# Kernel tuning notes

Measured on AMD Instinct MI355X. Metric: run time of the kernel, lower is better.

The kernel has to match this reference:

```python
import jax, jax.numpy as jnp
import numpy as np

EPS = 1e-5

def rmsnorm(x, g):
    var = jnp.mean(jnp.square(x), axis=-1, keepdims=True)
    return x * jax.lax.rsqrt(var + EPS) * g

def setup_inputs() -> dict:
    key = jax.random.key(0)
    ks = jax.random.split(key, 8)
    B, S, T, D = 2, 2048, 2048, 1024
    H, HKV, HD = 16, 4, 64
    std = 0.02
    return {
        "x": jax.random.normal(ks[0], (B, S, D), jnp.float32),
        "kv": jax.random.normal(ks[1], (B, T, D), jnp.float32),
        "wq": jax.random.normal(ks[2], (H * HD, D), jnp.float32) * std,
        "wk": jax.random.normal(ks[3], (HKV * HD, D), jnp.float32) * std,
        "wv": jax.random.normal(ks[4], (HKV * HD, D), jnp.float32) * std,
        "wo": jax.random.normal(ks[5], (D, H * HD), jnp.float32) * std,
        "gq": jnp.ones((D,), jnp.float32),
        "gkv": jnp.ones((D,), jnp.float32),
    }

def reference(x, kv, wq, wk, wv, wo, gq, gkv):
    B, S, D = x.shape
    T = kv.shape[1]
    H, HKV, HD = 16, 4, 64
    R = H // HKV  # heads per kv group
    xn = rmsnorm(x, gq)
    kvn = rmsnorm(kv, gkv)
    # projections
    q = (xn @ wq.T).reshape(B, S, HKV, R, HD)   # grouped query heads
    k = (kvn @ wk.T).reshape(B, T, HKV, HD)
    v = (kvn @ wv.T).reshape(B, T, HKV, HD)
    scale = 1.0 / jnp.sqrt(jnp.float32(HD))
    # block-mask is None -> full dense cross attention; GQA via broadcast einsum
    scores = jnp.einsum('bsgrd,btgd->bgrst', q, k) * scale  # [B,HKV,R,S,T]
    probs = jax.nn.softmax(scores, axis=-1)
    out = jnp.einsum('bgrst,btgd->bsgrd', probs, v)  # [B,S,HKV,R,HD]
    out = out.reshape(B, S, H * HD) @ wo.T
    return x + out
```

## Files before the change

kernel.cpp:

```cpp
#include <hip/hip_runtime.h>

#define DEV __device__ __forceinline__

typedef __attribute__((ext_vector_type(8))) short frag8;
typedef __attribute__((ext_vector_type(8))) _Float16 h8;
typedef __attribute__((ext_vector_type(4))) float f32x4;

DEV unsigned short f2bf(float f) {
  union { float f; unsigned int u; } v; v.f = f;
  unsigned int r = v.u + 0x7fffu + ((v.u >> 16) & 1u);
  return (unsigned short)(r >> 16);
}

DEV unsigned short f2h(float f) {
  union { _Float16 h[2]; unsigned short u[2]; } v;
  v.h[0] = (_Float16)f;
  return v.u[0];
}

DEV unsigned int pack2h(float a, float b) {
  union { __fp16 __attribute__((ext_vector_type(2))) p; unsigned int u; } v;
  v.p = __builtin_amdgcn_cvt_pkrtz(a, b);
  return v.u;
}

DEV void async_load16(const void* g, void* l) {
  __builtin_amdgcn_global_load_lds(
      (const __attribute__((address_space(1))) void*)g,
      (__attribute__((address_space(3))) void*)l,
      16, 0, 0);
}

__global__ __launch_bounds__(256) void fused_cast(const float* __restrict__ wq,
                                                  const float* __restrict__ wk,
                                                  const float* __restrict__ wv,
                                                  const float* __restrict__ wo,
                                                  unsigned short* __restrict__ wqb,
                                                  unsigned short* __restrict__ wkvb,
                                                  unsigned short* __restrict__ wob,
                                                  float qscale) {
  const int b = blockIdx.x;
  const float* src;
  unsigned short* dst;
  float sc = 1.0f;
  int base;
  if (b < 1024) { src = wq; dst = wqb; sc = qscale; base = b; }
  else if (b < 1280) { src = wk; dst = wkvb; base = b - 1024; }
  else if (b < 1536) { src = wv; dst = wkvb + 262144; base = b - 1280; }
  else { src = wo; dst = wob; base = b - 1536; }
  const int i = (base * 256 + threadIdx.x) * 4;
  float4 v = *(const float4*)&src[i];
  ushort4 o;
  o.x = f2bf(v.x * sc); o.y = f2bf(v.y * sc);
  o.z = f2bf(v.z * sc); o.w = f2bf(v.w * sc);
  *(ushort4*)&dst[i] = o;
}

__global__ __launch_bounds__(256) void rmsnorm2(const float* __restrict__ x,
                                                const float* __restrict__ kv,
                                                const float* __restrict__ gq,
                                                const float* __restrict__ gkv,
                                                unsigned short* __restrict__ xn,
                                                unsigned short* __restrict__ kvn) {
  int row = blockIdx.x;
  const int tid = threadIdx.x;
  const float* src;
  const float* g;
  unsigned short* dst;
  if (row < 4096) { src = x; g = gq; dst = xn; }
  else { row -= 4096; src = kv; g = gkv; dst = kvn; }
  const float* xr = src + (size_t)row * 1024;
  float4 v = *(const float4*)&xr[tid * 4];
  float ss = v.x * v.x + v.y * v.y + v.z * v.z + v.w * v.w;
  ss += __shfl_xor(ss, 32); ss += __shfl_xor(ss, 16);
  ss += __shfl_xor(ss, 8);  ss += __shfl_xor(ss, 4);
  ss += __shfl_xor(ss, 2);  ss += __shfl_xor(ss, 1);
  __shared__ float red[4];
  if ((tid & 63) == 0) red[tid >> 6] = ss;
  __syncthreads();
  float tot = red[0] + red[1] + red[2] + red[3];
  float inv = rsqrtf(tot * (1.0f / 1024.0f) + 1e-5f);
  float4 gv = *(const float4*)&g[tid * 4];
  ushort4 o;
  o.x = f2bf(v.x * inv * gv.x); o.y = f2bf(v.y * inv * gv.y);
  o.z = f2bf(v.z * inv * gv.z); o.w = f2bf(v.w * inv * gv.w);
  *(ushort4*)&dst[(size_t)row * 1024 + tid * 4] = o;
}

template <int BM, int BN, int MODE>
__global__ __launch_bounds__(256) void gemm_bt(const unsigned short* __restrict__ A,
                                               const unsigned short* __restrict__ W,
                                               void* __restrict__ out,
                                               const float* __restrict__ resid,
                                               unsigned short* __restrict__ out2,
                                               int M, int N, int K) {
  constexpr int MI = BM / 32, NI = BN / 32;
  constexpr int PA = BM / 32, PB = BN / 32;
  __shared__ unsigned short Al[2][2][BM * 32];
  __shared__ unsigned short Bl[2][2][BN * 32];
  const int tid = threadIdx.x;
  const int w = tid >> 6, l = tid & 63;
  const int quad = l >> 4, ln = l & 15;
  const int m0 = blockIdx.y * BM, n0 = blockIdx.x * BN;
  const int wm0 = (w >> 1) * (MI * 16), wn0 = (w & 1) * (NI * 16);
  const int r4 = l >> 2;
  const int c4 = (l & 3) * 8;

  f32x4 acc[MI][NI] = {};

  auto stage = [&](int buf, int kk) {
#pragma unroll
    for (int j = 0; j < PA; ++j) {
      const int idx = w * PA + j;
      const int p = idx / (BM / 16), c = idx % (BM / 16);
      async_load16(A + (size_t)(m0 + c * 16 + r4) * K + kk + p * 32 + c4,
                   &Al[buf][p][c * 512]);
    }
#pragma unroll
    for (int j = 0; j < PB; ++j) {
      const int idx = w * PB + j;
      const int p = idx / (BN / 16), c = idx % (BN / 16);
      async_load16(W + (size_t)(n0 + c * 16 + r4) * K + kk + p * 32 + c4,
                   &Bl[buf][p][c * 512]);
    }
  };

  stage(0, 0);
  const int iters = K >> 6;
#pragma unroll 2
  for (int it = 0; it < iters; ++it) {
    const int buf = it & 1;
    __syncthreads();
    if (it + 1 < iters) stage(buf ^ 1, (it + 1) << 6);
#pragma unroll
    for (int kc = 0; kc < 2; ++kc) {
      frag8 af[MI], bfr[NI];
#pragma unroll
      for (int mi = 0; mi < MI; ++mi)
        af[mi] = *(const frag8*)&Al[buf][kc][(wm0 + mi * 16 + ln) * 32 + quad * 8];
#pragma unroll
      for (int ni = 0; ni < NI; ++ni)
        bfr[ni] = *(const frag8*)&Bl[buf][kc][(wn0 + ni * 16 + ln) * 32 + quad * 8];
#pragma unroll
      for (int mi = 0; mi < MI; ++mi)
#pragma unroll
        for (int ni = 0; ni < NI; ++ni)
          acc[mi][ni] = __builtin_amdgcn_mfma_f32_16x16x32_bf16(af[mi], bfr[ni], acc[mi][ni], 0, 0, 0);
    }
  }

#pragma unroll
  for (int mi = 0; mi < MI; ++mi) {
#pragma unroll
    for (int ni = 0; ni < NI; ++ni) {
#pragma unroll
      for (int r = 0; r < 4; ++r) {
        const int row = m0 + wm0 + mi * 16 + quad * 4 + r;
        const int col = n0 + wn0 + ni * 16 + ln;
        const float v = acc[mi][ni][r];
        if (MODE == 0) {
          ((unsigned short*)out)[(size_t)row * N + col] = f2bf(v);
        } else if (MODE == 2) {
          const size_t idx = (size_t)row * N + col;
          ((float*)out)[idx] = resid[idx] + v;
        } else {
          if (col < 256) {
            ((unsigned short*)out)[(size_t)row * 256 + col] = f2bf(v);
          } else {
            const int c2 = col - 256, gg = c2 >> 6, dd = c2 & 63;
            const int bb = row >> 11, t = row & 2047;
            out2[((size_t)((bb * 4 + gg) * 64 + dd) << 11) + t] = f2h(v);
          }
        }
      }
    }
  }
}

__global__ __launch_bounds__(256) void flash_attn(const unsigned short* __restrict__ q,
                                                  const unsigned short* __restrict__ k,
                                                  const unsigned short* __restrict__ vT,
                                                  unsigned short* __restrict__ att) {
  __shared__ unsigned short KV[2][4][64 * 32];
  __shared__ unsigned short P[4 * 32 * 72];
  __shared__ float Lbuf[128];

  const int tid = threadIdx.x;
  const int w = tid >> 6, l = tid & 63;
  const int quad = l >> 4, ln = l & 15;
  const int s0 = blockIdx.x * 128;
  const int h = blockIdx.y, g = h >> 2, b = blockIdx.z;

  frag8 qf[2][2];
#pragma unroll
  for (int nq = 0; nq < 2; ++nq)
#pragma unroll
    for (int c = 0; c < 2; ++c)
      qf[nq][c] = *(const frag8*)&q[(((size_t)(b * 2048 + s0 + w * 32 + nq * 16 + ln)) << 10) +
                                    h * 64 + c * 32 + quad * 8];

  f32x4 oacc[2][4] = {};
  float lsum[2] = {0.0f, 0.0f};

  const unsigned short* kbase = k + ((size_t)(b * 2048)) * 256 + g * 64;
  const unsigned short* vbase = vT + (((size_t)(b * 4 + g) * 64) << 11);
  unsigned short* Pw = &P[w * 32 * 72];

  const int r4 = l >> 2;
  const int c4 = (l & 3) * 8;

  auto stage = [&](int buf, int t0) {
#pragma unroll
    for (int c = 0; c < 4; ++c) {
      const unsigned short* src;
      if (w < 2)
        src = kbase + (size_t)(t0 + c * 16 + r4) * 256 + w * 32 + c4;
      else
        src = vbase + (((size_t)(c * 16 + r4)) << 11) + t0 + (w - 2) * 32 + c4;
      async_load16(src, &KV[buf][w][c * 512]);
    }
  };

  stage(0, 0);
#pragma unroll 2
  for (int it = 0; it < 32; ++it) {
    const int buf = it & 1;
    __syncthreads();
    if (it < 31) stage(buf ^ 1, (it + 1) * 64);

    f32x4 st[2][4];
#pragma unroll
    for (int tb = 0; tb < 4; ++tb) {
      frag8 ka = *(const frag8*)&KV[buf][0][(tb * 16 + ln) * 32 + quad * 8];
      frag8 kb2 = *(const frag8*)&KV[buf][1][(tb * 16 + ln) * 32 + quad * 8];
#pragma unroll
      for (int nq = 0; nq < 2; ++nq) {
        f32x4 s = {};
        s = __builtin_amdgcn_mfma_f32_16x16x32_bf16(ka, qf[nq][0], s, 0, 0, 0);
        s = __builtin_amdgcn_mfma_f32_16x16x32_bf16(kb2, qf[nq][1], s, 0, 0, 0);
        st[nq][tb] = s;
      }
    }

#pragma unroll
    for (int nq = 0; nq < 2; ++nq) {
#pragma unroll
      for (int tb = 0; tb < 4; ++tb) {
        float p0 = __builtin_amdgcn_exp2f(fminf(st[nq][tb][0], 14.0f));
        float p1 = __builtin_amdgcn_exp2f(fminf(st[nq][tb][1], 14.0f));
        float p2 = __builtin_amdgcn_exp2f(fminf(st[nq][tb][2], 14.0f));
        float p3 = __builtin_amdgcn_exp2f(fminf(st[nq][tb][3], 14.0f));
        lsum[nq] += (p0 + p1) + (p2 + p3);
        uint2 pk; pk.x = pack2h(p0, p1); pk.y = pack2h(p2, p3);
        *(uint2*)&Pw[(nq * 16 + ln) * 72 + tb * 16 + quad * 4] = pk;
      }
    }

    asm volatile("s_waitcnt lgkmcnt(0)" ::: "memory");

#pragma unroll
    for (int c = 0; c < 2; ++c) {
      h8 pf0 = *(const h8*)&Pw[(0 * 16 + ln) * 72 + c * 32 + quad * 8];
      h8 pf1 = *(const h8*)&Pw[(1 * 16 + ln) * 72 + c * 32 + quad * 8];
#pragma unroll
      for (int cb = 0; cb < 4; ++cb) {
        h8 vb = *(const h8*)&KV[buf][2 + c][(cb * 16 + ln) * 32 + quad * 8];
        oacc[0][cb] = __builtin_amdgcn_mfma_f32_16x16x32_f16(pf0, vb, oacc[0][cb], 0, 0, 0);
        oacc[1][cb] = __builtin_amdgcn_mfma_f32_16x16x32_f16(pf1, vb, oacc[1][cb], 0, 0, 0);
      }
    }
  }

#pragma unroll
  for (int nq = 0; nq < 2; ++nq) {
    lsum[nq] += __shfl_xor(lsum[nq], 16);
    lsum[nq] += __shfl_xor(lsum[nq], 32);
    if (l < 16) Lbuf[w * 32 + nq * 16 + l] = 1.0f / lsum[nq];
  }
  __syncthreads();
#pragma unroll
  for (int nq = 0; nq < 2; ++nq) {
#pragma unroll
    for (int r = 0; r < 4; ++r) {
      const float inv = Lbuf[w * 32 + nq * 16 + quad * 4 + r];
      const size_t row = (size_t)(b * 2048 + s0 + w * 32 + nq * 16 + quad * 4 + r);
#pragma unroll
      for (int cb = 0; cb < 4; ++cb)
        att[(row << 10) + h * 64 + cb * 16 + ln] = f2bf(oacc[nq][cb][r] * inv);
    }
  }
}

extern "C" void kernel_launch(void* const* d_in, const int* in_sizes, int n_in,
                              void* d_out, int out_size, void* d_ws, size_t ws_size,
                              hipStream_t stream) {
  const float* x   = (const float*)d_in[0];
  const float* kv  = (const float*)d_in[1];
  const float* wq  = (const float*)d_in[2];
  const float* wk  = (const float*)d_in[3];
  const float* wv  = (const float*)d_in[4];
  const float* wo  = (const float*)d_in[5];
  const float* gq  = (const float*)d_in[6];
  const float* gkv = (const float*)d_in[7];

  char* ws = (char*)d_ws;
  unsigned short* xn   = (unsigned short*)(ws);
  unsigned short* kvn  = (unsigned short*)(ws + 8388608);
  unsigned short* qb   = (unsigned short*)(ws + 16777216);
  unsigned short* kb   = (unsigned short*)(ws + 25165824);
  unsigned short* vTb  = (unsigned short*)(ws + 27262976);
  unsigned short* attb = (unsigned short*)(ws + 29360128);
  unsigned short* wqb  = (unsigned short*)(ws + 37748736);
  unsigned short* wkvb = (unsigned short*)(ws + 39845888);
  unsigned short* wob  = (unsigned short*)(ws + 40894464);

  const float qscale = 0.18033688011112042f;
  fused_cast<<<2560, 256, 0, stream>>>(wq, wk, wv, wo, wqb, wkvb, wob, qscale);
  rmsnorm2<<<8192, 256, 0, stream>>>(x, kv, gq, gkv, xn, kvn);

  gemm_bt<128, 64, 0><<<dim3(16, 32), 256, 0, stream>>>(xn, wqb, qb, nullptr, nullptr,
                                                        4096, 1024, 1024);
  gemm_bt<64, 64, 3><<<dim3(8, 64), 256, 0, stream>>>(kvn, wkvb, kb, nullptr, vTb,
                                                      4096, 512, 1024);

  flash_attn<<<dim3(16, 16, 2), 256, 0, stream>>>(qb, kb, vTb, attb);

  gemm_bt<128, 64, 2><<<dim3(16, 32), 256, 0, stream>>>(attb, wob, d_out, x, nullptr,
                                                        4096, 1024, 1024);
}
```

Baseline: 211.8 us.

## Split attention over key halves with combine kernel; single-buffer KV; smaller GEMM tiles

Flash attention now splits the key dimension into two halves across the grid z-axis, which doubles the block count from 512 to 1024. Each half writes unnormalized fp16 partial outputs and row sums into reused workspace, and a new combine kernel sums the halves and normalizes. The KV shared buffer drops from double-buffered async prefetch to a single buffer with a sync before and after each load, and launch bounds now request higher occupancy. The Q and output GEMMs switch to 64x64 tiles for more blocks. The costs are an extra kernel launch, extra partial-output traffic, lost load/compute overlap inside attention, and fp16 range risk on the unnormalized sums.

```diff
diff --git a/kernel.cpp b/kernel.cpp
--- a/kernel.cpp
+++ b/kernel.cpp
@@ -16,6 +16,12 @@
   union { _Float16 h[2]; unsigned short u[2]; } v;
   v.h[0] = (_Float16)f;
   return v.u[0];
+}
+
+DEV float h2f(unsigned short u) {
+  union { _Float16 h[2]; unsigned short u[2]; } v;
+  v.u[0] = u;
+  return (float)v.h[0];
 }
 
 DEV unsigned int pack2h(float a, float b) {
@@ -177,19 +183,26 @@
   }
 }
 
-__global__ __launch_bounds__(256) void flash_attn(const unsigned short* __restrict__ q,
-                                                  const unsigned short* __restrict__ k,
-                                                  const unsigned short* __restrict__ vT,
-                                                  unsigned short* __restrict__ att) {
-  __shared__ unsigned short KV[2][4][64 * 32];
+__global__ __launch_bounds__(256, 4) void flash_attn(const unsigned short* __restrict__ q,
+                                                     const unsigned short* __restrict__ k,
+                                                     const unsigned short* __restrict__ vT,
+                                                     unsigned short* __restrict__ o0,
+                                                     unsigned short* __restrict__ o1,
+                                                     float* __restrict__ l0p,
+                                                     float* __restrict__ l1p) {
+  __shared__ unsigned short KV[4][64 * 32];
   __shared__ unsigned short P[4 * 32 * 72];
-  __shared__ float Lbuf[128];
 
   const int tid = threadIdx.x;
   const int w = tid >> 6, l = tid & 63;
   const int quad = l >> 4, ln = l & 15;
   const int s0 = blockIdx.x * 128;
-  const int h = blockIdx.y, g = h >> 2, b = blockIdx.z;
+  const int h = blockIdx.y, g = h >> 2;
+  const int b = blockIdx.z >> 1, ts = blockIdx.z & 1;
+  const int tbase = ts << 10;
+
+  unsigned short* Opart = ts ? o1 : o0;
+  float* lpart = ts ? l1p : l0p;
 
   frag8 qf[2][2];
 #pragma unroll
@@ -209,7 +222,9 @@
   const int r4 = l >> 2;
   const int c4 = (l & 3) * 8;
 
-  auto stage = [&](int buf, int t0) {
+  for (int it = 0; it < 16; ++it) {
+    const int t0 = tbase + it * 64;
+    __syncthreads();
 #pragma unroll
     for (int c = 0; c < 4; ++c) {
       const unsigned short* src;
@@ -217,22 +232,15 @@
         src = kbase + (size_t)(t0 + c * 16 + r4) * 256 + w * 32 + c4;
       else
         src = vbase + (((size_t)(c * 16 + r4)) << 11) + t0 + (w - 2) * 32 + c4;
-      async_load16(src, &KV[buf][w][c * 512]);
-    }
-  };
-
-  stage(0, 0);
-#pragma unroll 2
-  for (int it = 0; it < 32; ++it) {
-    const int buf = it & 1;
+      async_load16(src, &KV[w][c * 512]);
+    }
     __syncthreads();
-    if (it < 31) stage(buf ^ 1, (it + 1) * 64);
 
     f32x4 st[2][4];
 #pragma unroll
     for (int tb = 0; tb < 4; ++tb) {
-      frag8 ka = *(const frag8*)&KV[buf][0][(tb * 16 + ln) * 32 + quad * 8];
-      frag8 kb2 = *(const frag8*)&KV[buf][1][(tb * 16 + ln) * 32 + quad * 8];
+      frag8 ka = *(const frag8*)&KV[0][(tb * 16 + ln) * 32 + quad * 8];
+      frag8 kb2 = *(const frag8*)&KV[1][(tb * 16 + ln) * 32 + quad * 8];
 #pragma unroll
       for (int nq = 0; nq < 2; ++nq) {
         f32x4 s = {};
@@ -264,7 +272,7 @@
       h8 pf1 = *(const h8*)&Pw[(1 * 16 + ln) * 72 + c * 32 + quad * 8];
 #pragma unroll
       for (int cb = 0; cb < 4; ++cb) {
-        h8 vb = *(const h8*)&KV[buf][2 + c][(cb * 16 + ln) * 32 + quad * 8];
+        h8 vb = *(const h8*)&KV[2 + c][(cb * 16 + ln) * 32 + quad * 8];
         oacc[0][cb] = __builtin_amdgcn_mfma_f32_16x16x32_f16(pf0, vb, oacc[0][cb], 0, 0, 0);
         oacc[1][cb] = __builtin_amdgcn_mfma_f32_16x16x32_f16(pf1, vb, oacc[1][cb], 0, 0, 0);
       }
@@ -275,20 +283,36 @@
   for (int nq = 0; nq < 2; ++nq) {
     lsum[nq] += __shfl_xor(lsum[nq], 16);
     lsum[nq] += __shfl_xor(lsum[nq], 32);
-    if (l < 16) Lbuf[w * 32 + nq * 16 + l] = 1.0f / lsum[nq];
+    if (l < 16)
+      lpart[(size_t)(b * 2048 + s0 + w * 32 + nq * 16 + l) * 16 + h] = lsum[nq];
+#pragma unroll
+    for (int r = 0; r < 4; ++r) {
+      const size_t row = (size_t)(b * 2048 + s0 + w * 32 + nq * 16 + quad * 4 + r);
+#pragma unroll
+      for (int cb = 0; cb < 4; ++cb)
+        Opart[(row << 10) + h * 64 + cb * 16 + ln] = f2h(oacc[nq][cb][r]);
+    }
   }
-  __syncthreads();
-#pragma unroll
-  for (int nq = 0; nq < 2; ++nq) {
-#pragma unroll
-    for (int r = 0; r < 4; ++r) {
-      const float inv = Lbuf[w * 32 + nq * 16 + quad * 4 + r];
-      const size_t row = (size_t)(b * 2048 + s0 + w * 32 + nq * 16 + quad * 4 + r);
-#pragma unroll
-      for (int cb = 0; cb < 4; ++cb)
-        att[(row << 10) + h * 64 + cb * 16 + ln] = f2bf(oacc[nq][cb][r] * inv);
-    }
-  }
+}
+
+__global__ __launch_bounds__(256) void combine(const unsigned short* __restrict__ O0,
+                                               const unsigned short* __restrict__ O1,
+                                               const float* __restrict__ l0p,
+                                               const float* __restrict__ l1p,
+                                               unsigned short* __restrict__ att) {
+  const int row = blockIdx.x, tid = threadIdx.x;
+  const int col = tid * 4;
+  const int h = tid >> 4;
+  const float inv = 1.0f / (l0p[row * 16 + h] + l1p[row * 16 + h]);
+  const size_t idx = ((size_t)row << 10) + col;
+  ushort4 a = *(const ushort4*)&O0[idx];
+  ushort4 b = *(const ushort4*)&O1[idx];
+  ushort4 o;
+  o.x = f2bf((h2f(a.x) + h2f(b.x)) * inv);
+  o.y = f2bf((h2f(a.y) + h2f(b.y)) * inv);
+  o.z = f2bf((h2f(a.z) + h2f(b.z)) * inv);
+  o.w = f2bf((h2f(a.w) + h2f(b.w)) * inv);
+  *(ushort4*)&att[idx] = o;
 }
 
 extern "C" void kernel_launch(void* const* d_in, const int* in_sizes, int n_in,
@@ -313,18 +337,23 @@
   unsigned short* wqb  = (unsigned short*)(ws + 37748736);
   unsigned short* wkvb = (unsigned short*)(ws + 39845888);
   unsigned short* wob  = (unsigned short*)(ws + 40894464);
+  unsigned short* Opart0 = xn;
+  unsigned short* Opart1 = kvn;
+  float* l0p = (float*)wqb;
+  float* l1p = (float*)(ws + 37748736 + 262144);
 
   const float qscale = 0.18033688011112042f;
   fused_cast<<<2560, 256, 0, stream>>>(wq, wk, wv, wo, wqb, wkvb, wob, qscale);
   rmsnorm2<<<8192, 256, 0, stream>>>(x, kv, gq, gkv, xn, kvn);
 
-  gemm_bt<128, 64, 0><<<dim3(16, 32), 256, 0, stream>>>(xn, wqb, qb, nullptr, nullptr,
-                                                        4096, 1024, 1024);
+  gemm_bt<64, 64, 0><<<dim3(16, 64), 256, 0, stream>>>(xn, wqb, qb, nullptr, nullptr,
+                                                       4096, 1024, 1024);
   gemm_bt<64, 64, 3><<<dim3(8, 64), 256, 0, stream>>>(kvn, wkvb, kb, nullptr, vTb,
                                                       4096, 512, 1024);
 
-  flash_attn<<<dim3(16, 16, 2), 256, 0, stream>>>(qb, kb, vTb, attb);
-
-  gemm_bt<128, 64, 2><<<dim3(16, 32), 256, 0, stream>>>(attb, wob, d_out, x, nullptr,
-                                                        4096, 1024, 1024);
-}
+  flash_attn<<<dim3(16, 16, 4), 256, 0, stream>>>(qb, kb, vTb, Opart0, Opart1, l0p, l1p);
+  combine<<<4096, 256, 0, stream>>>(Opart0, Opart1, l0p, l1p, attb);
+
+  gemm_bt<64, 64, 2><<<dim3(16, 64), 256, 0, stream>>>(attb, wob, d_out, x, nullptr,
+                                                       4096, 1024, 1024);
+}
```

Measured after the change: 204.1 us. 3.7% less time.
